# Performance work log

Measured on AMD Instinct MI355X. Metric: run time of the kernel, lower is better.

## Reference

```python
import jax, jax.numpy as jnp
import numpy as np

B, H, W, C = 64, 32, 32, 256
HZ, WZ = 16, 16
N = 64          # hidden_dim = n_proposals
K = 3           # dynamic depthwise kernel size
EPS = 1e-5


def _layernorm(x, g, b):
    mu = jnp.mean(x, axis=-1, keepdims=True)
    var = jnp.var(x, axis=-1, keepdims=True)
    return (x - mu) * jax.lax.rsqrt(var + EPS) * g + b


def setup_inputs() -> dict:
    key = jax.random.key(0)
    ks = jax.random.split(key, 8)
    s = 0.02  # weight init scale
    return {
        "x_feat": jax.random.normal(ks[0], (B, H, W, C), jnp.float32),
        "z_feat": jax.random.normal(ks[1], (B, HZ, WZ, C), jnp.float32),
        "Wz": jax.random.normal(ks[2], (C, N), jnp.float32) * s,
        "bz": jnp.zeros((N,), jnp.float32),
        "Wx": jax.random.normal(ks[3], (C, N), jnp.float32) * s,
        "bx": jnp.zeros((N,), jnp.float32),
        "Wdyn": jax.random.normal(ks[4], (C, N + K), jnp.float32) * s,
        "bdyn": jnp.zeros((N + K,), jnp.float32),
        "g_norm": jnp.ones((C,), jnp.float32),
        "b_norm": jnp.zeros((C,), jnp.float32),
        "Wp": jax.random.normal(ks[5], (C, 1), jnp.float32) * s,
        "bp": jnp.zeros((1,), jnp.float32),
        "g_ln": jnp.ones((C,), jnp.float32),
        "b_ln": jnp.zeros((C,), jnp.float32),
    }


def _dysep_conv_atten(query, value, Wdyn, bdyn, g_norm, b_norm):
    # query, value: [B, N, C]
    dy = query @ Wdyn + bdyn                      # [B, N, N+K]
    w_depth = dy[:, :, :K]                        # [B, N, K] per-channel depthwise kernels
    w_point = dy[:, :, K:]                        # [B, N, N] per-sample pointwise (1x1) weights
    # depthwise conv along C with 'same' padding (torch conv1d = cross-correlation)
    vpad = jnp.pad(value, ((0, 0), (0, 0), (1, 1)))
    depth = (w_depth[..., 0:1] * vpad[:, :, 0:C]
             + w_depth[..., 1:2] * vpad[:, :, 1:C + 1]
             + w_depth[..., 2:3] * vpad[:, :, 2:C + 2])
    depth = jax.nn.relu(depth)                    # [B, N, C]
    point = jnp.einsum('bnm,bmc->bnc', w_point, depth)
    return _layernorm(point, g_norm, b_norm)


def reference(x_feat, z_feat, Wz, bz, Wx, bx, Wdyn, bdyn,
              g_norm, b_norm, Wp, bp, g_ln, b_ln):
    # kernels from template features (detached in the original: kernels.detach())
    z_core = z_feat @ Wz + bz                                   # [B,HZ,WZ,N]
    kernels = jnp.einsum('bhwn,bhwc->bnc', z_core, z_feat)      # [B,N,C]
    kernels = jax.lax.stop_gradient(kernels)

    x_n = x_feat @ Wx + bx                                      # [B,H,W,N]
    kernels_x = jnp.einsum('bhwn,bhwc->bnc', x_n, x_feat)       # [B,N,C]
    kernels_x = _dysep_conv_atten(kernels, kernels_x, Wdyn, bdyn, g_norm, b_norm)

    x_corr = jnp.einsum('bnc,bhwn->bhwc', kernels_x, x_n)       # [B,H,W,C]
    proto = kernels_x @ Wp + bp                                 # [B,N,1]
    tem = jax.nn.sigmoid(jnp.einsum('bnd,bnc->bdc', proto, kernels_x))  # [B,1,C]
    tem = tem[:, :, None, :]                                    # [B,1,1,C]
    x_corr = x_corr * tem

    return x_feat + jax.nn.relu(_layernorm(x_corr, g_ln, b_ln))
```

## Files before the change

kernel.cpp:

```cpp
#include <hip/hip_runtime.h>
#include <math.h>

#define EPSV 1e-5f

typedef __attribute__((ext_vector_type(8))) short short8;
typedef __attribute__((ext_vector_type(4))) float f32x4;

static __device__ __forceinline__ unsigned bfpack2(float lo, float hi) {
    union { float f; unsigned u; } a, b;
    a.f = lo; b.f = hi;
    unsigned ua = a.u + 0x7fffu + ((a.u >> 16) & 1u);
    unsigned ub = b.u + 0x7fffu + ((b.u >> 16) & 1u);
    return (ua >> 16) | (ub & 0xffff0000u);
}

__global__ __launch_bounds__(256) void gram(
    const float* __restrict__ Xx, const float* __restrict__ Xz,
    float* __restrict__ Gx, float* __restrict__ Gz,
    float* __restrict__ csx, float* __restrict__ csz)
{
    __shared__ __align__(16) unsigned short AT[128 * 72];
    __shared__ __align__(16) unsigned short BT[128 * 72];
    __shared__ float csr[8 * 128];
    int id = blockIdx.x;
    const float* X; float* G; float* cs; int P;
    if (id < 192) { X = Xx; G = Gx; cs = csx; P = 1024; }
    else { id -= 192; X = Xz; G = Gz; cs = csz; P = 256; }
    const int b = id & 63;
    const int tile = id >> 6;
    const int ci = (tile == 1) ? 1 : 0;
    const int cj = (tile == 0) ? 0 : 1;
    const bool diag = (tile < 2);
    const int nk = P >> 6;
    const int t = threadIdx.x;
    const int cq = (t & 31) * 4;
    const int ph = t >> 5;
    const float* Xb = X + (long)b * P * 256;

    const int w = t >> 6;
    const int wr = w >> 1, wc = w & 1;
    const int quad = (t >> 4) & 3, lane16 = t & 15;

    f32x4 acc[4][4] = {};
    float csA[4] = {0.f, 0.f, 0.f, 0.f};

    for (int kc = 0; kc < nk; ++kc) {
        const int p0 = kc * 64 + ph * 8;
        float4 va[8], vb[8];
#pragma unroll
        for (int k = 0; k < 8; ++k)
            va[k] = *(const float4*)(Xb + (long)(p0 + k) * 256 + ci * 128 + cq);
        if (!diag) {
#pragma unroll
            for (int k = 0; k < 8; ++k)
                vb[k] = *(const float4*)(Xb + (long)(p0 + k) * 256 + cj * 128 + cq);
        }
        __syncthreads();
#pragma unroll
        for (int j = 0; j < 4; ++j) {
            uint4 pk;
            pk.x = bfpack2(((const float*)&va[0])[j], ((const float*)&va[1])[j]);
            pk.y = bfpack2(((const float*)&va[2])[j], ((const float*)&va[3])[j]);
            pk.z = bfpack2(((const float*)&va[4])[j], ((const float*)&va[5])[j]);
            pk.w = bfpack2(((const float*)&va[6])[j], ((const float*)&va[7])[j]);
            *(uint4*)&AT[(cq + j) * 72 + ph * 8] = pk;
            if (diag) {
                csA[j] += ((const float*)&va[0])[j] + ((const float*)&va[1])[j]
                        + ((const float*)&va[2])[j] + ((const float*)&va[3])[j]
                        + ((const float*)&va[4])[j] + ((const float*)&va[5])[j]
                        + ((const float*)&va[6])[j] + ((const float*)&va[7])[j];
            }
        }
        if (!diag) {
#pragma unroll
            for (int j = 0; j < 4; ++j) {
                uint4 pk;
                pk.x = bfpack2(((const float*)&vb[0])[j], ((const float*)&vb[1])[j]);
                pk.y = bfpack2(((const float*)&vb[2])[j], ((const float*)&vb[3])[j]);
                pk.z = bfpack2(((const float*)&vb[4])[j], ((const float*)&vb[5])[j]);
                pk.w = bfpack2(((const float*)&vb[6])[j], ((const float*)&vb[7])[j]);
                *(uint4*)&BT[(cq + j) * 72 + ph * 8] = pk;
            }
        }
        __syncthreads();
        const unsigned short* Br = diag ? AT : BT;
#pragma unroll
        for (int ks = 0; ks < 2; ++ks) {
            const int ko = ks * 32 + quad * 8;
            short8 bfrag[4];
#pragma unroll
            for (int ni = 0; ni < 4; ++ni)
                bfrag[ni] = *(const short8*)&Br[(wc * 64 + ni * 16 + lane16) * 72 + ko];
#pragma unroll
            for (int mi = 0; mi < 4; ++mi) {
                short8 afrag = *(const short8*)&AT[(wr * 64 + mi * 16 + lane16) * 72 + ko];
#pragma unroll
                for (int ni = 0; ni < 4; ++ni)
                    acc[mi][ni] = __builtin_amdgcn_mfma_f32_16x16x32_bf16(afrag, bfrag[ni], acc[mi][ni], 0, 0, 0);
            }
        }
    }
#pragma unroll
    for (int mi = 0; mi < 4; ++mi) {
        const int rbase = ci * 128 + wr * 64 + mi * 16 + quad * 4;
#pragma unroll
        for (int ni = 0; ni < 4; ++ni) {
            const int col = cj * 128 + wc * 64 + ni * 16 + lane16;
#pragma unroll
            for (int r = 0; r < 4; ++r) {
                G[((long)(b * 256 + rbase + r)) * 256 + col] = acc[mi][ni][r];
                if (!diag)
                    G[((long)(b * 256 + col)) * 256 + rbase + r] = acc[mi][ni][r];
            }
        }
    }
    if (diag) {
#pragma unroll
        for (int j = 0; j < 4; ++j) csr[ph * 128 + cq + j] = csA[j];
        __syncthreads();
        if (t < 128) {
            float s = 0.f;
#pragma unroll
            for (int k = 0; k < 8; ++k) s += csr[k * 128 + t];
            cs[b * 256 + ci * 128 + t] = s;
        }
    }
}

__global__ __launch_bounds__(256) void proj(
    const float* __restrict__ Gx, const float* __restrict__ csx,
    const float* __restrict__ Wx, const float* __restrict__ bx,
    float* __restrict__ kxr,
    const float* __restrict__ Gz, const float* __restrict__ csz,
    const float* __restrict__ Wz, const float* __restrict__ bz,
    float* __restrict__ kern)
{
    __shared__ __align__(16) unsigned short ATW[64 * 264];
    __shared__ __align__(16) unsigned short BTC[64 * 72];
    const int t = threadIdx.x;
    const int id = blockIdx.x;
    const int b = id & 63, s = id >> 6;
    const float *G, *cs, *W, *bias; float* O;
    if (s < 4) { G = Gx; cs = csx; W = Wx; bias = bx; O = kxr; }
    else       { G = Gz; cs = csz; W = Wz; bias = bz; O = kern; }
    const int ct = s & 3;
    const int n = t & 63, ph = t >> 6;
#pragma unroll
    for (int cc = 0; cc < 4; ++cc) {
        float v[16];
#pragma unroll
        for (int k = 0; k < 16; ++k) v[k] = W[(ph * 64 + cc * 16 + k) * 64 + n];
        uint4 p0, p1;
        p0.x = bfpack2(v[0], v[1]);   p0.y = bfpack2(v[2], v[3]);
        p0.z = bfpack2(v[4], v[5]);   p0.w = bfpack2(v[6], v[7]);
        p1.x = bfpack2(v[8], v[9]);   p1.y = bfpack2(v[10], v[11]);
        p1.z = bfpack2(v[12], v[13]); p1.w = bfpack2(v[14], v[15]);
        *(uint4*)&ATW[n * 264 + ph * 64 + cc * 16]     = p0;
        *(uint4*)&ATW[n * 264 + ph * 64 + cc * 16 + 8] = p1;
    }
    const int row = t >> 2, cq = t & 3;
    const int w = t >> 6, quad = (t >> 4) & 3, lane16 = t & 15;
    const float* Grow = G + ((long)(b * 256 + ct * 64 + row)) * 256 + cq * 16;
    f32x4 acc[4] = {{0.f,0.f,0.f,0.f},{0.f,0.f,0.f,0.f},{0.f,0.f,0.f,0.f},{0.f,0.f,0.f,0.f}};
    for (int kc = 0; kc < 4; ++kc) {
        float4 g0 = *(const float4*)(Grow + kc * 64 + 0);
        float4 g1 = *(const float4*)(Grow + kc * 64 + 4);
        float4 g2 = *(const float4*)(Grow + kc * 64 + 8);
        float4 g3 = *(const float4*)(Grow + kc * 64 + 12);
        uint4 pk0, pk1;
        pk0.x = bfpack2(g0.x, g0.y); pk0.y = bfpack2(g0.z, g0.w);
        pk0.z = bfpack2(g1.x, g1.y); pk0.w = bfpack2(g1.z, g1.w);
        pk1.x = bfpack2(g2.x, g2.y); pk1.y = bfpack2(g2.z, g2.w);
        pk1.z = bfpack2(g3.x, g3.y); pk1.w = bfpack2(g3.z, g3.w);
        __syncthreads();
        *(uint4*)&BTC[row * 72 + cq * 16]     = pk0;
        *(uint4*)&BTC[row * 72 + cq * 16 + 8] = pk1;
        __syncthreads();
#pragma unroll
        for (int ks = 0; ks < 2; ++ks) {
            const int ko = ks * 32 + quad * 8;
            short8 bfrag = *(const short8*)&BTC[(w * 16 + lane16) * 72 + ko];
#pragma unroll
            for (int mi = 0; mi < 4; ++mi) {
                short8 afrag = *(const short8*)&ATW[(mi * 16 + lane16) * 264 + kc * 64 + ko];
                acc[mi] = __builtin_amdgcn_mfma_f32_16x16x32_bf16(afrag, bfrag, acc[mi], 0, 0, 0);
            }
        }
    }
    const int col = ct * 64 + w * 16 + lane16;
    const float csv = cs[b * 256 + col];
#pragma unroll
    for (int mi = 0; mi < 4; ++mi) {
        const int nrow = mi * 16 + quad * 4;
#pragma unroll
        for (int r = 0; r < 4; ++r)
            O[((long)(b * 64 + nrow + r)) * 256 + col] = acc[mi][r] + bias[nrow + r] * csv;
    }
}

__global__ __launch_bounds__(256) void dy_all(
    const float* __restrict__ kern, const float* __restrict__ Wdyn,
    const float* __restrict__ bdyn, float* __restrict__ dyb)
{
    __shared__ float Ac[16 * 64];
    __shared__ float Wc[16 * 64];
    __shared__ float Wd3[48];
    const int b = blockIdx.x, t = threadIdx.x;
    const int tr = t >> 4, tc = t & 15;
    float acc[4][4];
#pragma unroll
    for (int j = 0; j < 4; ++j) {
        float bj = bdyn[3 + tc * 4 + j];
        acc[0][j] = bj; acc[1][j] = bj; acc[2][j] = bj; acc[3][j] = bj;
    }
    const int lr = t >> 2, lc = (t & 3) * 4;
    const int wl = t >> 4, wj = (t & 15) * 4;
    const int nwd = t / 3, jwd = t - nwd * 3;
    float wdacc = 0.f;
    float4 av = *(const float4*)(kern + ((long)(b * 64 + lr)) * 256 + lc);
    float w0 = Wdyn[wl * 67 + 3 + wj + 0];
    float w1 = Wdyn[wl * 67 + 3 + wj + 1];
    float w2 = Wdyn[wl * 67 + 3 + wj + 2];
    float w3 = Wdyn[wl * 67 + 3 + wj + 3];
    float wdr = (t < 48) ? Wdyn[(t / 3) * 67 + (t % 3)] : 0.f;

    for (int c0 = 0; c0 < 256; c0 += 16) {
        Ac[(lc+0)*64 + lr] = av.x; Ac[(lc+1)*64 + lr] = av.y;
        Ac[(lc+2)*64 + lr] = av.z; Ac[(lc+3)*64 + lr] = av.w;
        Wc[wl*64 + wj+0] = w0; Wc[wl*64 + wj+1] = w1;
        Wc[wl*64 + wj+2] = w2; Wc[wl*64 + wj+3] = w3;
        if (t < 48) Wd3[t] = wdr;
        __syncthreads();
        if (c0 + 16 < 256) {
            av = *(const float4*)(kern + ((long)(b * 64 + lr)) * 256 + c0 + 16 + lc);
            w0 = Wdyn[(c0 + 16 + wl) * 67 + 3 + wj + 0];
            w1 = Wdyn[(c0 + 16 + wl) * 67 + 3 + wj + 1];
            w2 = Wdyn[(c0 + 16 + wl) * 67 + 3 + wj + 2];
            w3 = Wdyn[(c0 + 16 + wl) * 67 + 3 + wj + 3];
            if (t < 48) wdr = Wdyn[(c0 + 16 + t / 3) * 67 + (t % 3)];
        }
#pragma unroll
        for (int cl = 0; cl < 16; ++cl) {
            float4 a = *(float4*)&Ac[cl * 64 + tr * 4];
            float4 w = *(float4*)&Wc[cl * 64 + tc * 4];
            acc[0][0]+=a.x*w.x; acc[0][1]+=a.x*w.y; acc[0][2]+=a.x*w.z; acc[0][3]+=a.x*w.w;
            acc[1][0]+=a.y*w.x; acc[1][1]+=a.y*w.y; acc[1][2]+=a.y*w.z; acc[1][3]+=a.y*w.w;
            acc[2][0]+=a.z*w.x; acc[2][1]+=a.z*w.y; acc[2][2]+=a.z*w.z; acc[2][3]+=a.z*w.w;
            acc[3][0]+=a.w*w.x; acc[3][1]+=a.w*w.y; acc[3][2]+=a.w*w.z; acc[3][3]+=a.w*w.w;
        }
        if (t < 192) {
#pragma unroll
            for (int cl = 0; cl < 16; ++cl)
                wdacc += Ac[cl * 64 + nwd] * Wd3[cl * 3 + jwd];
        }
        __syncthreads();
    }
#pragma unroll
    for (int i = 0; i < 4; ++i) {
        float4 o = make_float4(acc[i][0], acc[i][1], acc[i][2], acc[i][3]);
        *(float4*)(dyb + ((long)(b * 64 + tr * 4 + i)) * 68 + tc * 4) = o;
    }
    if (t < 192) dyb[((long)(b * 64 + nwd)) * 68 + 64 + jwd] = wdacc + bdyn[jwd];
}

__global__ __launch_bounds__(256) void depthpoint(
    const float* __restrict__ dyb, const float* __restrict__ v,
    const float* __restrict__ g, const float* __restrict__ Wp,
    float* __restrict__ point, float* __restrict__ partials)
{
    __shared__ float smem[13312];
    float* wpT = smem;
    float* wd3 = smem + 4352;
    float* vt  = smem + 4608;
    float* dep = smem + 8960;
    float* rs  = vt;

    const int t = threadIdx.x;
    const int b = blockIdx.y, ct = blockIdx.x, c0 = ct * 64;
    const int tr = t >> 4, tc = t & 15;

#pragma unroll
    for (int i = 0; i < 4; ++i) {
        int idx = t + i * 256; int n = idx >> 4, m0 = (idx & 15) * 4;
        float4 w4 = *(const float4*)(dyb + ((long)(b * 64 + n)) * 68 + m0);
        wpT[(m0+0)*68 + n] = w4.x; wpT[(m0+1)*68 + n] = w4.y;
        wpT[(m0+2)*68 + n] = w4.z; wpT[(m0+3)*68 + n] = w4.w;
    }
    if (t < 64) {
        long o = ((long)(b * 64 + t)) * 68 + 64;
        wd3[t*4+0] = dyb[o+0]; wd3[t*4+1] = dyb[o+1]; wd3[t*4+2] = dyb[o+2];
    }
    {
        int m = t >> 2, lc0 = (t & 3) * 17;
#pragma unroll
        for (int k = 0; k < 17; ++k) {
            int lc = lc0 + k;
            if (lc < 66) {
                int c = c0 - 1 + lc;
                vt[m * 68 + lc] = (c >= 0 && c < 256) ? v[((long)(b * 64 + m)) * 256 + c] : 0.f;
            }
        }
    }
    __syncthreads();
#pragma unroll
    for (int im = 0; im < 4; ++im) {
        int m = tr * 4 + im;
        float w0 = wd3[m*4+0], w1 = wd3[m*4+1], w2 = wd3[m*4+2];
#pragma unroll
        for (int jc = 0; jc < 4; ++jc) {
            int cl = tc * 4 + jc;
            float d = w0 * vt[m*68 + cl] + w1 * vt[m*68 + cl + 1] + w2 * vt[m*68 + cl + 2];
            dep[m*68 + cl] = fmaxf(d, 0.f);
        }
    }
    __syncthreads();
    float acc[4][4] = {};
#pragma unroll 16
    for (int m = 0; m < 64; ++m) {
        float4 a4 = *(float4*)&wpT[m * 68 + tr * 4];
        float4 d4 = *(float4*)&dep[m * 68 + tc * 4];
        acc[0][0]+=a4.x*d4.x; acc[0][1]+=a4.x*d4.y; acc[0][2]+=a4.x*d4.z; acc[0][3]+=a4.x*d4.w;
        acc[1][0]+=a4.y*d4.x; acc[1][1]+=a4.y*d4.y; acc[1][2]+=a4.y*d4.z; acc[1][3]+=a4.y*d4.w;
        acc[2][0]+=a4.z*d4.x; acc[2][1]+=a4.z*d4.y; acc[2][2]+=a4.z*d4.z; acc[2][3]+=a4.z*d4.w;
        acc[3][0]+=a4.w*d4.x; acc[3][1]+=a4.w*d4.y; acc[3][2]+=a4.w*d4.z; acc[3][3]+=a4.w*d4.w;
    }
    int cg = c0 + tc * 4;
    float4 g4  = *(const float4*)(g + cg);
    float4 wp4 = *(const float4*)(Wp + cg);
    float gw0 = g4.x*wp4.x, gw1 = g4.y*wp4.y, gw2 = g4.z*wp4.z, gw3 = g4.w*wp4.w;
#pragma unroll
    for (int i = 0; i < 4; ++i) {
        float4 o = make_float4(acc[i][0], acc[i][1], acc[i][2], acc[i][3]);
        *(float4*)(point + ((long)(b * 64 + tr * 4 + i)) * 256 + cg) = o;
        float s  = o.x + o.y + o.z + o.w;
        float s2 = o.x*o.x + o.y*o.y + o.z*o.z + o.w*o.w;
        float dg = o.x*gw0 + o.y*gw1 + o.z*gw2 + o.w*gw3;
        rs[0*1088 + (tr*4+i)*17 + tc] = s;
        rs[1*1088 + (tr*4+i)*17 + tc] = s2;
        rs[2*1088 + (tr*4+i)*17 + tc] = dg;
    }
    __syncthreads();
    if (t < 64) {
        float s = 0.f, s2 = 0.f, dg = 0.f;
#pragma unroll
        for (int j = 0; j < 16; ++j) {
            s  += rs[t*17 + j];
            s2 += rs[1088 + t*17 + j];
            dg += rs[2176 + t*17 + j];
        }
        long base = ((long)(b * 4 + ct)) * 192;
        partials[base + t]        = s;
        partials[base + 64 + t]   = s2;
        partials[base + 128 + t]  = dg;
    }
}

__global__ __launch_bounds__(256) void lntem(
    const float* __restrict__ partials, const float* __restrict__ point,
    const float* __restrict__ g, const float* __restrict__ bta,
    const float* __restrict__ Wp, const float* __restrict__ bp,
    float* __restrict__ murr, float* __restrict__ AB)
{
    __shared__ float sA[256], sB[256];
    __shared__ float wnv[64];
    __shared__ float tot[4];
    const int b = blockIdx.x, t = threadIdx.x;
    const int c = t;
    float gc = g[c], bc = bta[c], wpc = Wp[c];
    sA[t] = gc * wpc; sB[t] = bc * wpc;
    __syncthreads();
    for (int off = 128; off >= 1; off >>= 1) {
        if (t < off) { sA[t] += sA[t+off]; sB[t] += sB[t+off]; }
        __syncthreads();
    }
    if (t == 0) { tot[0] = sA[0]; tot[1] = sB[0] + bp[0]; }
    __syncthreads();
    float Sgw = tot[0], Sbw = tot[1];

    float protoe = 0.f, mu = 0.f, rr = 0.f;
    if (t < 64) {
        float S1 = 0.f, S2 = 0.f, Sdg = 0.f;
#pragma unroll
        for (int ct = 0; ct < 4; ++ct) {
            long o = ((long)(b * 4 + ct)) * 192;
            S1 += partials[o + t]; S2 += partials[o + 64 + t]; Sdg += partials[o + 128 + t];
        }
        mu = S1 * (1.f / 256.f);
        float var = S2 * (1.f / 256.f) - mu * mu;
        rr = rsqrtf(var + EPSV);
        protoe = rr * (Sdg - mu * Sgw) + Sbw;
        wnv[t] = protoe * rr;
        murr[b * 128 + 2*t]     = rr;
        murr[b * 128 + 2*t + 1] = -mu * rr;
    }
    __syncthreads();
    sA[t] = (t < 64) ? protoe * rr * mu : 0.f;
    sB[t] = (t < 64) ? protoe : 0.f;
    __syncthreads();
    for (int off = 128; off >= 1; off >>= 1) {
        if (t < off) { sA[t] += sA[t+off]; sB[t] += sB[t+off]; }
        __syncthreads();
    }
    if (t == 0) { tot[2] = sA[0]; tot[3] = sB[0]; }
    __syncthreads();
    float Bv = tot[2], Sv = tot[3];

    const float* pcol = point + (long)b * 64 * 256 + c;
    float a0 = 0.f, a1 = 0.f, a2 = 0.f, a3 = 0.f;
#pragma unroll
    for (int n = 0; n < 64; n += 4) {
        a0 += wnv[n+0] * pcol[(n+0) * 256];
        a1 += wnv[n+1] * pcol[(n+1) * 256];
        a2 += wnv[n+2] * pcol[(n+2) * 256];
        a3 += wnv[n+3] * pcol[(n+3) * 256];
    }
    float accA = a0 + a1 + a2 + a3;
    float x = gc * (accA - Bv) + bc * Sv;
    float temv = 1.f / (1.f + expf(-x));
    AB[b * 512 + c]       = gc * temv;
    AB[b * 512 + 256 + c] = bc * temv;
}

__global__ __launch_bounds__(256) void buildM(
    const float* __restrict__ point, const float* __restrict__ murr,
    const float* __restrict__ AB, const float* __restrict__ Wx,
    const float* __restrict__ bx,
    unsigned short* __restrict__ MT, float* __restrict__ svec)
{
    __shared__ float ks_s[64 * 68];
    __shared__ float wt_s[64 * 68];
    const int t = threadIdx.x;
    const int id = blockIdx.x;
    const int b = id & 63, mt = id >> 6;
    {
        const int n = t >> 2, q = t & 3;
        const float rn = murr[b * 128 + 2 * n], qn = murr[b * 128 + 2 * n + 1];
        const float* prow = point + ((long)(b * 64 + n)) * 256 + mt * 64 + q * 16;
        const float* Arow = AB + b * 512 + mt * 64 + q * 16;
#pragma unroll
        for (int j = 0; j < 4; ++j) {
            float4 p4 = *(const float4*)(prow + j * 4);
            float4 A4 = *(const float4*)(Arow + j * 4);
            float4 B4 = *(const float4*)(Arow + 256 + j * 4);
            float4 kv;
            kv.x = (p4.x * rn + qn) * A4.x + B4.x;
            kv.y = (p4.y * rn + qn) * A4.y + B4.y;
            kv.z = (p4.z * rn + qn) * A4.z + B4.z;
            kv.w = (p4.w * rn + qn) * A4.w + B4.w;
            *(float4*)&ks_s[n * 68 + q * 16 + j * 4] = kv;
        }
    }
    __syncthreads();
    if (t < 64) {
        float sv = 0.f;
#pragma unroll
        for (int n2 = 0; n2 < 64; ++n2) sv += bx[n2] * ks_s[n2 * 68 + t];
        svec[b * 256 + mt * 64 + t] = sv;
    }
    const int tr = t >> 4, tc = t & 15;
    const int nw = t & 63, ph = t >> 6;
    for (int cc = 0; cc < 4; ++cc) {
        float wv[16];
#pragma unroll
        for (int k = 0; k < 16; ++k) wv[k] = Wx[(cc * 64 + ph * 16 + k) * 64 + nw];
        __syncthreads();
#pragma unroll
        for (int k = 0; k < 16; ++k) wt_s[nw * 68 + ph * 16 + k] = wv[k];
        __syncthreads();
        float a2[4][4] = {};
#pragma unroll 16
        for (int n2 = 0; n2 < 64; ++n2) {
            float4 a4 = *(float4*)&ks_s[n2 * 68 + tr * 4];
            float4 w4 = *(float4*)&wt_s[n2 * 68 + tc * 4];
            a2[0][0]+=a4.x*w4.x; a2[0][1]+=a4.x*w4.y; a2[0][2]+=a4.x*w4.z; a2[0][3]+=a4.x*w4.w;
            a2[1][0]+=a4.y*w4.x; a2[1][1]+=a4.y*w4.y; a2[1][2]+=a4.y*w4.z; a2[1][3]+=a4.y*w4.w;
            a2[2][0]+=a4.z*w4.x; a2[2][1]+=a4.z*w4.y; a2[2][2]+=a4.z*w4.z; a2[2][3]+=a4.z*w4.w;
            a2[3][0]+=a4.w*w4.x; a2[3][1]+=a4.w*w4.y; a2[3][2]+=a4.w*w4.z; a2[3][3]+=a4.w*w4.w;
        }
#pragma unroll
        for (int i = 0; i < 4; ++i) {
            uint2 pk;
            pk.x = bfpack2(a2[i][0], a2[i][1]);
            pk.y = bfpack2(a2[i][2], a2[i][3]);
            *(uint2*)&MT[((long)(b * 256 + mt * 64 + tr * 4 + i)) * 256 + cc * 64 + tc * 4] = pk;
        }
    }
}

__global__ __launch_bounds__(256) void final2(
    const float* __restrict__ xf, const unsigned short* __restrict__ MT,
    const float* __restrict__ svec, const float* __restrict__ g,
    const float* __restrict__ bt, float* __restrict__ out)
{
    __shared__ __align__(16) float SlArr[32 * 132];
    __shared__ float red1[128], red2[128];
    __shared__ float muS[32], rrS[32];
    unsigned short* XT = (unsigned short*)SlArr;
    float* Sl = SlArr;
    const int t = threadIdx.x;
    const int id = blockIdx.x;
    const int b = id & 63, pt = id >> 6;
    const int w = t >> 6, quad = (t >> 4) & 3, lane16 = t & 15;
    const float* Xb = xf + ((long)(b * 1024 + pt * 32)) * 256;
    {
        const int p = t >> 3, q = t & 7;
#pragma unroll
        for (int i = 0; i < 8; ++i) {
            const int c = q * 32 + i * 4;
            float4 v = *(const float4*)(Xb + (long)p * 256 + c);
            uint2 pk;
            pk.x = bfpack2(v.x, v.y);
            pk.y = bfpack2(v.z, v.w);
            *(uint2*)&XT[p * 264 + c] = pk;
        }
    }
    __syncthreads();
    f32x4 acc[2][4] = {};
    const unsigned short* Mb = MT + (long)b * 65536;
    for (int ks = 0; ks < 8; ++ks) {
        const int ko = ks * 32 + quad * 8;
        short8 bf4[4], af2[2];
#pragma unroll
        for (int ni = 0; ni < 4; ++ni)
            bf4[ni] = *(const short8*)(Mb + (long)(w * 64 + ni * 16 + lane16) * 256 + ko);
#pragma unroll
        for (int mi = 0; mi < 2; ++mi)
            af2[mi] = *(const short8*)&XT[(mi * 16 + lane16) * 264 + ko];
#pragma unroll
        for (int mi = 0; mi < 2; ++mi)
#pragma unroll
            for (int ni = 0; ni < 4; ++ni)
                acc[mi][ni] = __builtin_amdgcn_mfma_f32_16x16x32_bf16(af2[mi], bf4[ni], acc[mi][ni], 0, 0, 0);
    }
    float sv4[4];
#pragma unroll
    for (int ni = 0; ni < 4; ++ni) sv4[ni] = svec[b * 256 + w * 64 + ni * 16 + lane16];
#pragma unroll
    for (int mi = 0; mi < 2; ++mi)
#pragma unroll
        for (int r = 0; r < 4; ++r) {
            float s1 = 0.f, s2 = 0.f;
#pragma unroll
            for (int ni = 0; ni < 4; ++ni) {
                float v2 = acc[mi][ni][r] + sv4[ni];
                acc[mi][ni][r] = v2;
                s1 += v2; s2 += v2 * v2;
            }
#pragma unroll
            for (int m = 1; m <= 8; m <<= 1) {
                s1 += __shfl_xor(s1, m);
                s2 += __shfl_xor(s2, m);
            }
            if (lane16 == 0) {
                red1[(mi * 16 + quad * 4 + r) * 4 + w] = s1;
                red2[(mi * 16 + quad * 4 + r) * 4 + w] = s2;
            }
        }
    __syncthreads();
    if (t < 32) {
        float sa = red1[t*4] + red1[t*4+1] + red1[t*4+2] + red1[t*4+3];
        float sb = red2[t*4] + red2[t*4+1] + red2[t*4+2] + red2[t*4+3];
        float m = sa * (1.f / 256.f);
        muS[t] = m;
        rrS[t] = rsqrtf(sb * (1.f / 256.f) - m * m + EPSV);
    }
#pragma unroll
    for (int h = 0; h < 2; ++h) {
        __syncthreads();
        if ((w >> 1) == h) {
            const int chalf = (w & 1) * 64;
#pragma unroll
            for (int mi = 0; mi < 2; ++mi)
#pragma unroll
                for (int ni = 0; ni < 4; ++ni)
#pragma unroll
                    for (int r = 0; r < 4; ++r)
                        Sl[(mi * 16 + quad * 4 + r) * 132 + chalf + ni * 16 + lane16] = acc[mi][ni][r];
        }
        __syncthreads();
        {
            const int p = t >> 3, q = t & 7;
            const float m = muS[p], rr = rrS[p];
            const long grow = ((long)(b * 1024 + pt * 32 + p)) * 256;
#pragma unroll
            for (int j = 0; j < 4; ++j) {
                const int cl = q * 16 + j * 4;
                const int c = h * 128 + cl;
                float4 a  = *(float4*)&Sl[p * 132 + cl];
                float4 g4 = *(const float4*)(g + c);
                float4 b4 = *(const float4*)(bt + c);
                float4 xv = *(const float4*)(xf + grow + c);
                float4 o;
                o.x = xv.x + fmaxf((a.x - m) * rr * g4.x + b4.x, 0.f);
                o.y = xv.y + fmaxf((a.y - m) * rr * g4.y + b4.y, 0.f);
                o.z = xv.z + fmaxf((a.z - m) * rr * g4.z + b4.z, 0.f);
                o.w = xv.w + fmaxf((a.w - m) * rr * g4.w + b4.w, 0.f);
                *(float4*)(out + grow + c) = o;
            }
        }
    }
}

extern "C" void kernel_launch(void* const* d_in, const int* in_sizes, int n_in,
                              void* d_out, int out_size, void* d_ws, size_t ws_size,
                              hipStream_t stream)
{
    (void)in_sizes; (void)n_in; (void)out_size; (void)ws_size;
    const float* x_feat = (const float*)d_in[0];
    const float* z_feat = (const float*)d_in[1];
    const float* Wz     = (const float*)d_in[2];
    const float* bz     = (const float*)d_in[3];
    const float* Wx     = (const float*)d_in[4];
    const float* bx     = (const float*)d_in[5];
    const float* Wdyn   = (const float*)d_in[6];
    const float* bdyn   = (const float*)d_in[7];
    const float* g_norm = (const float*)d_in[8];
    const float* b_norm = (const float*)d_in[9];
    const float* Wp     = (const float*)d_in[10];
    const float* bp     = (const float*)d_in[11];
    const float* g_ln   = (const float*)d_in[12];
    const float* b_ln   = (const float*)d_in[13];
    float* out = (float*)d_out;

    float* ws       = (float*)d_ws;
    float* Gx       = ws;
    float* Gz       = Gx + 4194304;
    float* kern     = Gz + 4194304;
    float* kxr      = kern + 1048576;
    float* point    = kxr + 1048576;
    float* dyb      = point + 1048576;
    float* partials = dyb + 278528;
    float* murr     = partials + 49152;
    float* AB       = murr + 8192;
    float* csx      = AB + 32768;
    float* csz      = csx + 16384;
    float* svec     = csz + 16384;
    unsigned short* MT = (unsigned short*)(svec + 16384);

    gram<<<384, 256, 0, stream>>>(x_feat, z_feat, Gx, Gz, csx, csz);
    proj<<<512, 256, 0, stream>>>(Gx, csx, Wx, bx, kxr, Gz, csz, Wz, bz, kern);
    dy_all<<<64, 256, 0, stream>>>(kern, Wdyn, bdyn, dyb);
    depthpoint<<<dim3(4, 64), 256, 0, stream>>>(dyb, kxr, g_norm, Wp, point, partials);
    lntem<<<64, 256, 0, stream>>>(partials, point, g_norm, b_norm, Wp, bp, murr, AB);
    buildM<<<256, 256, 0, stream>>>(point, murr, AB, Wx, bx, MT, svec);
    final2<<<2048, 256, 0, stream>>>(x_feat, MT, svec, g_ln, b_ln, out);
}
```

Before: 297.8 us.

## Store Gram matrices in bf16, fuse dynamic-weight GEMM into proj, swizzle gram LDS

Gram kernel now runs 512 threads with XOR-swizzled LDS tiles and writes bf16 Gram matrices, splitting the off-diagonal tile so each half-block writes one orientation instead of transposed scattered stores. Proj reads bf16 G fragments directly into registers, dropping the LDS staging and syncs. The z-path now also computes per-channel-slice partial products with Wdyn, which removes the serial 64-block dy_all kernel, and depthpoint sums the four partials plus bias. final2 prefetches the next MT fragments one step ahead. The aim is to cut memory traffic and a kernel launch, at the cost of extra bf16 rounding of G and extra partial-buffer traffic.

After: 280.0 us. -6.0%, faster.

```diff
diff --git a/kernel.cpp b/kernel.cpp
--- a/kernel.cpp
+++ b/kernel.cpp
@@ -13,258 +13,274 @@
     unsigned ub = b.u + 0x7fffu + ((b.u >> 16) & 1u);
     return (ua >> 16) | (ub & 0xffff0000u);
 }
-
-__global__ __launch_bounds__(256) void gram(
+static __device__ __forceinline__ unsigned short bf1(float v) {
+    return (unsigned short)bfpack2(v, 0.f);
+}
+
+__global__ __launch_bounds__(512) void gram(
     const float* __restrict__ Xx, const float* __restrict__ Xz,
-    float* __restrict__ Gx, float* __restrict__ Gz,
+    unsigned short* __restrict__ Gx, unsigned short* __restrict__ Gz,
     float* __restrict__ csx, float* __restrict__ csz)
 {
     __shared__ __align__(16) unsigned short AT[128 * 72];
     __shared__ __align__(16) unsigned short BT[128 * 72];
-    __shared__ float csr[8 * 128];
-    int id = blockIdx.x;
-    const float* X; float* G; float* cs; int P;
-    if (id < 192) { X = Xx; G = Gx; cs = csx; P = 1024; }
-    else { id -= 192; X = Xz; G = Gz; cs = csz; P = 256; }
+    __shared__ float csr[16 * 128];
+    const int id = blockIdx.x;
     const int b = id & 63;
-    const int tile = id >> 6;
-    const int ci = (tile == 1) ? 1 : 0;
-    const int cj = (tile == 0) ? 0 : 1;
+    const int path = (id >> 6) & 1;
+    const int tile = id >> 7;
     const bool diag = (tile < 2);
+    const int ci = diag ? tile : 0;
+    const float* X = path ? Xz : Xx;
+    unsigned short* G = (path ? Gz : Gx) + (long)b * 65536;
+    float* cs = path ? csz : csx;
+    const int P = path ? 256 : 1024;
     const int nk = P >> 6;
     const int t = threadIdx.x;
     const int cq = (t & 31) * 4;
     const int ph = t >> 5;
+    const int w = t >> 6;
+    const int quad = (t >> 4) & 3, lane16 = t & 15;
     const float* Xb = X + (long)b * P * 256;
-
-    const int w = t >> 6;
-    const int wr = w >> 1, wc = w & 1;
-    const int quad = (t >> 4) & 3, lane16 = t & 15;
+    const int colA = ci * 128;
 
     f32x4 acc[4][4] = {};
     float csA[4] = {0.f, 0.f, 0.f, 0.f};
 
     for (int kc = 0; kc < nk; ++kc) {
-        const int p0 = kc * 64 + ph * 8;
-        float4 va[8], vb[8];
-#pragma unroll
-        for (int k = 0; k < 8; ++k)
-            va[k] = *(const float4*)(Xb + (long)(p0 + k) * 256 + ci * 128 + cq);
+        const int p0 = kc * 64 + ph * 4;
+        float4 va[4], vb[4];
+#pragma unroll
+        for (int k = 0; k < 4; ++k)
+            va[k] = *(const float4*)(Xb + (long)(p0 + k) * 256 + colA + cq);
         if (!diag) {
 #pragma unroll
-            for (int k = 0; k < 8; ++k)
-                vb[k] = *(const float4*)(Xb + (long)(p0 + k) * 256 + cj * 128 + cq);
+            for (int k = 0; k < 4; ++k)
+                vb[k] = *(const float4*)(Xb + (long)(p0 + k) * 256 + 128 + cq);
         }
         __syncthreads();
 #pragma unroll
         for (int j = 0; j < 4; ++j) {
-            uint4 pk;
+            const int row = cq + j;
+            const int key = (row >> 2) & 7;
+            uint2 pk;
             pk.x = bfpack2(((const float*)&va[0])[j], ((const float*)&va[1])[j]);
             pk.y = bfpack2(((const float*)&va[2])[j], ((const float*)&va[3])[j]);
-            pk.z = bfpack2(((const float*)&va[4])[j], ((const float*)&va[5])[j]);
-            pk.w = bfpack2(((const float*)&va[6])[j], ((const float*)&va[7])[j]);
-            *(uint4*)&AT[(cq + j) * 72 + ph * 8] = pk;
-            if (diag) {
+            *(uint2*)&AT[row * 72 + (((ph >> 1) ^ key) << 3) + ((ph & 1) << 2)] = pk;
+            if (diag)
                 csA[j] += ((const float*)&va[0])[j] + ((const float*)&va[1])[j]
-                        + ((const float*)&va[2])[j] + ((const float*)&va[3])[j]
-                        + ((const float*)&va[4])[j] + ((const float*)&va[5])[j]
-                        + ((const float*)&va[6])[j] + ((const float*)&va[7])[j];
-            }
+                        + ((const float*)&va[2])[j] + ((const float*)&va[3])[j];
         }
         if (!diag) {
 #pragma unroll
             for (int j = 0; j < 4; ++j) {
-                uint4 pk;
+                const int row = cq + j;
+                const int key = (row >> 2) & 7;
+                uint2 pk;
                 pk.x = bfpack2(((const float*)&vb[0])[j], ((const float*)&vb[1])[j]);
                 pk.y = bfpack2(((const float*)&vb[2])[j], ((const float*)&vb[3])[j]);
-                pk.z = bfpack2(((const float*)&vb[4])[j], ((const float*)&vb[5])[j]);
-                pk.w = bfpack2(((const float*)&vb[6])[j], ((const float*)&vb[7])[j]);
-                *(uint4*)&BT[(cq + j) * 72 + ph * 8] = pk;
-            }
-        }
-        __syncthreads();
-        const unsigned short* Br = diag ? AT : BT;
-#pragma unroll
-        for (int ks = 0; ks < 2; ++ks) {
-            const int ko = ks * 32 + quad * 8;
-            short8 bfrag[4];
-#pragma unroll
-            for (int ni = 0; ni < 4; ++ni)
-                bfrag[ni] = *(const short8*)&Br[(wc * 64 + ni * 16 + lane16) * 72 + ko];
-#pragma unroll
-            for (int mi = 0; mi < 4; ++mi) {
-                short8 afrag = *(const short8*)&AT[(wr * 64 + mi * 16 + lane16) * 72 + ko];
-#pragma unroll
-                for (int ni = 0; ni < 4; ++ni)
-                    acc[mi][ni] = __builtin_amdgcn_mfma_f32_16x16x32_bf16(afrag, bfrag[ni], acc[mi][ni], 0, 0, 0);
-            }
-        }
-    }
-#pragma unroll
-    for (int mi = 0; mi < 4; ++mi) {
-        const int rbase = ci * 128 + wr * 64 + mi * 16 + quad * 4;
-#pragma unroll
-        for (int ni = 0; ni < 4; ++ni) {
-            const int col = cj * 128 + wc * 64 + ni * 16 + lane16;
-#pragma unroll
-            for (int r = 0; r < 4; ++r) {
-                G[((long)(b * 256 + rbase + r)) * 256 + col] = acc[mi][ni][r];
-                if (!diag)
-                    G[((long)(b * 256 + col)) * 256 + rbase + r] = acc[mi][ni][r];
+                *(uint2*)&BT[row * 72 + (((ph >> 1) ^ key) << 3) + ((ph & 1) << 2)] = pk;
+            }
+        }
+        __syncthreads();
+        if (diag) {
+            const int wr = w >> 2, wc4 = w & 3;
+#pragma unroll
+            for (int ks = 0; ks < 2; ++ks) {
+                const int slot = ks * 4 + quad;
+                short8 bfr[2];
+#pragma unroll
+                for (int ni = 0; ni < 2; ++ni) {
+                    const int rw = wc4 * 32 + ni * 16 + lane16;
+                    bfr[ni] = *(const short8*)&AT[rw * 72 + ((slot ^ ((rw >> 2) & 7)) << 3)];
+                }
+#pragma unroll
+                for (int mi = 0; mi < 4; ++mi) {
+                    const int ra = wr * 64 + mi * 16 + lane16;
+                    short8 afr = *(const short8*)&AT[ra * 72 + ((slot ^ ((ra >> 2) & 7)) << 3)];
+#pragma unroll
+                    for (int ni = 0; ni < 2; ++ni)
+                        acc[mi][ni] = __builtin_amdgcn_mfma_f32_16x16x32_bf16(afr, bfr[ni], acc[mi][ni], 0, 0, 0);
+                }
+            }
+        } else {
+            const int sel = w >> 2, w2 = w & 3, wr = w2 >> 1, wc = w2 & 1;
+            const unsigned short* As = sel ? BT : AT;
+            const unsigned short* Bs = sel ? AT : BT;
+#pragma unroll
+            for (int ks = 0; ks < 2; ++ks) {
+                const int slot = ks * 4 + quad;
+                short8 bfr[4];
+#pragma unroll
+                for (int ni = 0; ni < 4; ++ni) {
+                    const int rw = wc * 64 + ni * 16 + lane16;
+                    bfr[ni] = *(const short8*)&Bs[rw * 72 + ((slot ^ ((rw >> 2) & 7)) << 3)];
+                }
+#pragma unroll
+                for (int mi = 0; mi < 4; ++mi) {
+                    const int ra = wr * 64 + mi * 16 + lane16;
+                    short8 afr = *(const short8*)&As[ra * 72 + ((slot ^ ((ra >> 2) & 7)) << 3)];
+#pragma unroll
+                    for (int ni = 0; ni < 4; ++ni)
+                        acc[mi][ni] = __builtin_amdgcn_mfma_f32_16x16x32_bf16(afr, bfr[ni], acc[mi][ni], 0, 0, 0);
+                }
             }
         }
     }
     if (diag) {
+        const int wr = w >> 2, wc4 = w & 3;
+#pragma unroll
+        for (int mi = 0; mi < 4; ++mi) {
+            const int rbase = ci * 128 + wr * 64 + mi * 16 + quad * 4;
+#pragma unroll
+            for (int ni = 0; ni < 2; ++ni) {
+                const int col = ci * 128 + wc4 * 32 + ni * 16 + lane16;
+#pragma unroll
+                for (int r = 0; r < 4; ++r)
+                    G[(rbase + r) * 256 + col] = bf1(acc[mi][ni][r]);
+            }
+        }
 #pragma unroll
         for (int j = 0; j < 4; ++j) csr[ph * 128 + cq + j] = csA[j];
         __syncthreads();
         if (t < 128) {
             float s = 0.f;
 #pragma unroll
-            for (int k = 0; k < 8; ++k) s += csr[k * 128 + t];
+            for (int k = 0; k < 16; ++k) s += csr[k * 128 + t];
             cs[b * 256 + ci * 128 + t] = s;
         }
+    } else {
+        const int sel = w >> 2, w2 = w & 3, wr = w2 >> 1, wc = w2 & 1;
+        const int R = sel ? 128 : 0, C = sel ? 0 : 128;
+#pragma unroll
+        for (int mi = 0; mi < 4; ++mi) {
+            const int rbase = R + wr * 64 + mi * 16 + quad * 4;
+#pragma unroll
+            for (int ni = 0; ni < 4; ++ni) {
+                const int col = C + wc * 64 + ni * 16 + lane16;
+#pragma unroll
+                for (int r = 0; r < 4; ++r)
+                    G[(rbase + r) * 256 + col] = bf1(acc[mi][ni][r]);
+            }
+        }
     }
 }
 
 __global__ __launch_bounds__(256) void proj(
-    const float* __restrict__ Gx, const float* __restrict__ csx,
+    const unsigned short* __restrict__ Gx, const float* __restrict__ csx,
     const float* __restrict__ Wx, const float* __restrict__ bx,
     float* __restrict__ kxr,
-    const float* __restrict__ Gz, const float* __restrict__ csz,
+    const unsigned short* __restrict__ Gz, const float* __restrict__ csz,
     const float* __restrict__ Wz, const float* __restrict__ bz,
-    float* __restrict__ kern)
+    const float* __restrict__ Wdyn, float* __restrict__ dypart)
 {
     __shared__ __align__(16) unsigned short ATW[64 * 264];
-    __shared__ __align__(16) unsigned short BTC[64 * 72];
+    __shared__ float SLICE[64 * 68];
+    __shared__ float WC2[64 * 68];
+    __shared__ float WD3L[192];
     const int t = threadIdx.x;
     const int id = blockIdx.x;
     const int b = id & 63, s = id >> 6;
-    const float *G, *cs, *W, *bias; float* O;
-    if (s < 4) { G = Gx; cs = csx; W = Wx; bias = bx; O = kxr; }
-    else       { G = Gz; cs = csz; W = Wz; bias = bz; O = kern; }
+    const bool xp = (s < 4);
     const int ct = s & 3;
-    const int n = t & 63, ph = t >> 6;
+    const unsigned short* G = xp ? Gx : Gz;
+    const float* cs   = xp ? csx : csz;
+    const float* W    = xp ? Wx : Wz;
+    const float* bias = xp ? bx : bz;
+    const int n = t & 63, ph2 = t >> 6;
 #pragma unroll
     for (int cc = 0; cc < 4; ++cc) {
         float v[16];
 #pragma unroll
-        for (int k = 0; k < 16; ++k) v[k] = W[(ph * 64 + cc * 16 + k) * 64 + n];
+        for (int k = 0; k < 16; ++k) v[k] = W[(ph2 * 64 + cc * 16 + k) * 64 + n];
         uint4 p0, p1;
         p0.x = bfpack2(v[0], v[1]);   p0.y = bfpack2(v[2], v[3]);
         p0.z = bfpack2(v[4], v[5]);   p0.w = bfpack2(v[6], v[7]);
         p1.x = bfpack2(v[8], v[9]);   p1.y = bfpack2(v[10], v[11]);
         p1.z = bfpack2(v[12], v[13]); p1.w = bfpack2(v[14], v[15]);
-        *(uint4*)&ATW[n * 264 + ph * 64 + cc * 16]     = p0;
-        *(uint4*)&ATW[n * 264 + ph * 64 + cc * 16 + 8] = p1;
-    }
-    const int row = t >> 2, cq = t & 3;
+        *(uint4*)&ATW[n * 264 + ph2 * 64 + cc * 16]     = p0;
+        *(uint4*)&ATW[n * 264 + ph2 * 64 + cc * 16 + 8] = p1;
+    }
+    __syncthreads();
     const int w = t >> 6, quad = (t >> 4) & 3, lane16 = t & 15;
-    const float* Grow = G + ((long)(b * 256 + ct * 64 + row)) * 256 + cq * 16;
+    const unsigned short* Grow =
+        G + (long)(b * 256 + ct * 64 + w * 16 + lane16) * 256 + quad * 8;
+    short8 bfr[8];
+#pragma unroll
+    for (int u = 0; u < 8; ++u) bfr[u] = *(const short8*)(Grow + u * 32);
     f32x4 acc[4] = {{0.f,0.f,0.f,0.f},{0.f,0.f,0.f,0.f},{0.f,0.f,0.f,0.f},{0.f,0.f,0.f,0.f}};
-    for (int kc = 0; kc < 4; ++kc) {
-        float4 g0 = *(const float4*)(Grow + kc * 64 + 0);
-        float4 g1 = *(const float4*)(Grow + kc * 64 + 4);
-        float4 g2 = *(const float4*)(Grow + kc * 64 + 8);
-        float4 g3 = *(const float4*)(Grow + kc * 64 + 12);
-        uint4 pk0, pk1;
-        pk0.x = bfpack2(g0.x, g0.y); pk0.y = bfpack2(g0.z, g0.w);
-        pk0.z = bfpack2(g1.x, g1.y); pk0.w = bfpack2(g1.z, g1.w);
-        pk1.x = bfpack2(g2.x, g2.y); pk1.y = bfpack2(g2.z, g2.w);
-        pk1.z = bfpack2(g3.x, g3.y); pk1.w = bfpack2(g3.z, g3.w);
-        __syncthreads();
-        *(uint4*)&BTC[row * 72 + cq * 16]     = pk0;
-        *(uint4*)&BTC[row * 72 + cq * 16 + 8] = pk1;
-        __syncthreads();
+#pragma unroll
+    for (int kc = 0; kc < 4; ++kc)
 #pragma unroll
         for (int ks = 0; ks < 2; ++ks) {
             const int ko = ks * 32 + quad * 8;
-            short8 bfrag = *(const short8*)&BTC[(w * 16 + lane16) * 72 + ko];
+            const short8 bfrag = bfr[kc * 2 + ks];
 #pragma unroll
             for (int mi = 0; mi < 4; ++mi) {
                 short8 afrag = *(const short8*)&ATW[(mi * 16 + lane16) * 264 + kc * 64 + ko];
                 acc[mi] = __builtin_amdgcn_mfma_f32_16x16x32_bf16(afrag, bfrag, acc[mi], 0, 0, 0);
             }
         }
-    }
     const int col = ct * 64 + w * 16 + lane16;
     const float csv = cs[b * 256 + col];
-#pragma unroll
-    for (int mi = 0; mi < 4; ++mi) {
-        const int nrow = mi * 16 + quad * 4;
-#pragma unroll
-        for (int r = 0; r < 4; ++r)
-            O[((long)(b * 64 + nrow + r)) * 256 + col] = acc[mi][r] + bias[nrow + r] * csv;
-    }
-}
-
-__global__ __launch_bounds__(256) void dy_all(
-    const float* __restrict__ kern, const float* __restrict__ Wdyn,
-    const float* __restrict__ bdyn, float* __restrict__ dyb)
-{
-    __shared__ float Ac[16 * 64];
-    __shared__ float Wc[16 * 64];
-    __shared__ float Wd3[48];
-    const int b = blockIdx.x, t = threadIdx.x;
-    const int tr = t >> 4, tc = t & 15;
-    float acc[4][4];
-#pragma unroll
-    for (int j = 0; j < 4; ++j) {
-        float bj = bdyn[3 + tc * 4 + j];
-        acc[0][j] = bj; acc[1][j] = bj; acc[2][j] = bj; acc[3][j] = bj;
-    }
-    const int lr = t >> 2, lc = (t & 3) * 4;
-    const int wl = t >> 4, wj = (t & 15) * 4;
-    const int nwd = t / 3, jwd = t - nwd * 3;
-    float wdacc = 0.f;
-    float4 av = *(const float4*)(kern + ((long)(b * 64 + lr)) * 256 + lc);
-    float w0 = Wdyn[wl * 67 + 3 + wj + 0];
-    float w1 = Wdyn[wl * 67 + 3 + wj + 1];
-    float w2 = Wdyn[wl * 67 + 3 + wj + 2];
-    float w3 = Wdyn[wl * 67 + 3 + wj + 3];
-    float wdr = (t < 48) ? Wdyn[(t / 3) * 67 + (t % 3)] : 0.f;
-
-    for (int c0 = 0; c0 < 256; c0 += 16) {
-        Ac[(lc+0)*64 + lr] = av.x; Ac[(lc+1)*64 + lr] = av.y;
-        Ac[(lc+2)*64 + lr] = av.z; Ac[(lc+3)*64 + lr] = av.w;
-        Wc[wl*64 + wj+0] = w0; Wc[wl*64 + wj+1] = w1;
-        Wc[wl*64 + wj+2] = w2; Wc[wl*64 + wj+3] = w3;
-        if (t < 48) Wd3[t] = wdr;
-        __syncthreads();
-        if (c0 + 16 < 256) {
-            av = *(const float4*)(kern + ((long)(b * 64 + lr)) * 256 + c0 + 16 + lc);
-            w0 = Wdyn[(c0 + 16 + wl) * 67 + 3 + wj + 0];
-            w1 = Wdyn[(c0 + 16 + wl) * 67 + 3 + wj + 1];
-            w2 = Wdyn[(c0 + 16 + wl) * 67 + 3 + wj + 2];
-            w3 = Wdyn[(c0 + 16 + wl) * 67 + 3 + wj + 3];
-            if (t < 48) wdr = Wdyn[(c0 + 16 + t / 3) * 67 + (t % 3)];
-        }
-#pragma unroll
-        for (int cl = 0; cl < 16; ++cl) {
-            float4 a = *(float4*)&Ac[cl * 64 + tr * 4];
-            float4 w = *(float4*)&Wc[cl * 64 + tc * 4];
-            acc[0][0]+=a.x*w.x; acc[0][1]+=a.x*w.y; acc[0][2]+=a.x*w.z; acc[0][3]+=a.x*w.w;
-            acc[1][0]+=a.y*w.x; acc[1][1]+=a.y*w.y; acc[1][2]+=a.y*w.z; acc[1][3]+=a.y*w.w;
-            acc[2][0]+=a.z*w.x; acc[2][1]+=a.z*w.y; acc[2][2]+=a.z*w.z; acc[2][3]+=a.z*w.w;
-            acc[3][0]+=a.w*w.x; acc[3][1]+=a.w*w.y; acc[3][2]+=a.w*w.z; acc[3][3]+=a.w*w.w;
+    if (xp) {
+#pragma unroll
+        for (int mi = 0; mi < 4; ++mi) {
+            const int nrow = mi * 16 + quad * 4;
+#pragma unroll
+            for (int r = 0; r < 4; ++r)
+                kxr[((long)(b * 64 + nrow + r)) * 256 + col] = acc[mi][r] + bias[nrow + r] * csv;
+        }
+    } else {
+        const int cloc = w * 16 + lane16;
+#pragma unroll
+        for (int mi = 0; mi < 4; ++mi) {
+            const int nrow = mi * 16 + quad * 4;
+#pragma unroll
+            for (int r = 0; r < 4; ++r)
+                SLICE[cloc * 68 + nrow + r] = acc[mi][r] + bias[nrow + r] * csv;
+        }
+        {
+            const int m = t & 63, clg = t >> 6;
+#pragma unroll
+            for (int j = 0; j < 16; ++j) {
+                const int cl = clg * 16 + j;
+                WC2[cl * 68 + m] = Wdyn[((long)(ct * 64 + cl)) * 67 + 3 + m];
+            }
+            if (t < 192) WD3L[t] = Wdyn[((long)(ct * 64 + t / 3)) * 67 + (t % 3)];
+        }
+        __syncthreads();
+        const int tr = t >> 4, tc = t & 15;
+        float adv[4][4] = {};
+#pragma unroll 16
+        for (int cl = 0; cl < 64; ++cl) {
+            float4 a  = *(float4*)&SLICE[cl * 68 + tr * 4];
+            float4 wv = *(float4*)&WC2[cl * 68 + tc * 4];
+            adv[0][0]+=a.x*wv.x; adv[0][1]+=a.x*wv.y; adv[0][2]+=a.x*wv.z; adv[0][3]+=a.x*wv.w;
+            adv[1][0]+=a.y*wv.x; adv[1][1]+=a.y*wv.y; adv[1][2]+=a.y*wv.z; adv[1][3]+=a.y*wv.w;
+            adv[2][0]+=a.z*wv.x; adv[2][1]+=a.z*wv.y; adv[2][2]+=a.z*wv.z; adv[2][3]+=a.z*wv.w;
+            adv[3][0]+=a.w*wv.x; adv[3][1]+=a.w*wv.y; adv[3][2]+=a.w*wv.z; adv[3][3]+=a.w*wv.w;
+        }
+        const long base = (long)(b * 4 + ct) * 64;
+#pragma unroll
+        for (int i = 0; i < 4; ++i) {
+            float4 o = make_float4(adv[i][0], adv[i][1], adv[i][2], adv[i][3]);
+            *(float4*)(dypart + (base + tr * 4 + i) * 68 + tc * 4) = o;
         }
         if (t < 192) {
-#pragma unroll
-            for (int cl = 0; cl < 16; ++cl)
-                wdacc += Ac[cl * 64 + nwd] * Wd3[cl * 3 + jwd];
-        }
-        __syncthreads();
-    }
-#pragma unroll
-    for (int i = 0; i < 4; ++i) {
-        float4 o = make_float4(acc[i][0], acc[i][1], acc[i][2], acc[i][3]);
-        *(float4*)(dyb + ((long)(b * 64 + tr * 4 + i)) * 68 + tc * 4) = o;
-    }
-    if (t < 192) dyb[((long)(b * 64 + nwd)) * 68 + 64 + jwd] = wdacc + bdyn[jwd];
+            const int nwd3 = t / 3, jwd3 = t - nwd3 * 3;
+            float wdacc = 0.f;
+#pragma unroll 16
+            for (int cl = 0; cl < 64; ++cl)
+                wdacc += SLICE[cl * 68 + nwd3] * WD3L[cl * 3 + jwd3];
+            dypart[(base + nwd3) * 68 + 64 + jwd3] = wdacc;
+        }
+    }
 }
 
 __global__ __launch_bounds__(256) void depthpoint(
-    const float* __restrict__ dyb, const float* __restrict__ v,
+    const float* __restrict__ dyp, const float* __restrict__ bdyn,
+    const float* __restrict__ v,
     const float* __restrict__ g, const float* __restrict__ Wp,
     float* __restrict__ point, float* __restrict__ partials)
 {
@@ -282,13 +298,26 @@
 #pragma unroll
     for (int i = 0; i < 4; ++i) {
         int idx = t + i * 256; int n = idx >> 4, m0 = (idx & 15) * 4;
-        float4 w4 = *(const float4*)(dyb + ((long)(b * 64 + n)) * 68 + m0);
+        float4 a0 = *(const float4*)(dyp + ((long)((b * 4 + 0) * 64 + n)) * 68 + m0);
+        float4 a1 = *(const float4*)(dyp + ((long)((b * 4 + 1) * 64 + n)) * 68 + m0);
+        float4 a2 = *(const float4*)(dyp + ((long)((b * 4 + 2) * 64 + n)) * 68 + m0);
+        float4 a3 = *(const float4*)(dyp + ((long)((b * 4 + 3) * 64 + n)) * 68 + m0);
+        float4 w4;
+        w4.x = a0.x + a1.x + a2.x + a3.x + bdyn[3 + m0 + 0];
+        w4.y = a0.y + a1.y + a2.y + a3.y + bdyn[3 + m0 + 1];
+        w4.z = a0.z + a1.z + a2.z + a3.z + bdyn[3 + m0 + 2];
+        w4.w = a0.w + a1.w + a2.w + a3.w + bdyn[3 + m0 + 3];
         wpT[(m0+0)*68 + n] = w4.x; wpT[(m0+1)*68 + n] = w4.y;
         wpT[(m0+2)*68 + n] = w4.z; wpT[(m0+3)*68 + n] = w4.w;
     }
     if (t < 64) {
-        long o = ((long)(b * 64 + t)) * 68 + 64;
-        wd3[t*4+0] = dyb[o+0]; wd3[t*4+1] = dyb[o+1]; wd3[t*4+2] = dyb[o+2];
+        long o0 = ((long)((b * 4 + 0) * 64 + t)) * 68 + 64;
+        long o1 = ((long)((b * 4 + 1) * 64 + t)) * 68 + 64;
+        long o2 = ((long)((b * 4 + 2) * 64 + t)) * 68 + 64;
+        long o3 = ((long)((b * 4 + 3) * 64 + t)) * 68 + 64;
+#pragma unroll
+        for (int j = 0; j < 3; ++j)
+            wd3[t*4+j] = dyp[o0+j] + dyp[o1+j] + dyp[o2+j] + dyp[o3+j] + bdyn[j];
     }
     {
         int m = t >> 2, lc0 = (t & 3) * 17;
@@ -516,13 +545,20 @@
     }
     __syncthreads();
     f32x4 acc[2][4] = {};
-    const unsigned short* Mb = MT + (long)b * 65536;
+    const unsigned short* Mb = MT + (long)b * 65536 + quad * 8;
+    short8 bf4[4];
+#pragma unroll
+    for (int ni = 0; ni < 4; ++ni)
+        bf4[ni] = *(const short8*)(Mb + (long)(w * 64 + ni * 16 + lane16) * 256);
     for (int ks = 0; ks < 8; ++ks) {
         const int ko = ks * 32 + quad * 8;
-        short8 bf4[4], af2[2];
-#pragma unroll
-        for (int ni = 0; ni < 4; ++ni)
-            bf4[ni] = *(const short8*)(Mb + (long)(w * 64 + ni * 16 + lane16) * 256 + ko);
+        short8 nbf[4];
+        if (ks + 1 < 8) {
+#pragma unroll
+            for (int ni = 0; ni < 4; ++ni)
+                nbf[ni] = *(const short8*)(Mb + (long)(w * 64 + ni * 16 + lane16) * 256 + (ks + 1) * 32);
+        }
+        short8 af2[2];
 #pragma unroll
         for (int mi = 0; mi < 2; ++mi)
             af2[mi] = *(const short8*)&XT[(mi * 16 + lane16) * 264 + ko];
@@ -531,6 +567,8 @@
 #pragma unroll
             for (int ni = 0; ni < 4; ++ni)
                 acc[mi][ni] = __builtin_amdgcn_mfma_f32_16x16x32_bf16(af2[mi], bf4[ni], acc[mi][ni], 0, 0, 0);
+#pragma unroll
+        for (int ni = 0; ni < 4; ++ni) bf4[ni] = nbf[ni];
     }
     float sv4[4];
 #pragma unroll
@@ -623,24 +661,24 @@
     float* out = (float*)d_out;
 
     float* ws       = (float*)d_ws;
-    float* Gx       = ws;
-    float* Gz       = Gx + 4194304;
-    float* kern     = Gz + 4194304;
-    float* kxr      = kern + 1048576;
+    float* kxr      = ws;
     float* point    = kxr + 1048576;
-    float* dyb      = point + 1048576;
-    float* partials = dyb + 278528;
+    float* dypart   = point + 1048576;
+    float* partials = dypart + 1114112;
     float* murr     = partials + 49152;
     float* AB       = murr + 8192;
     float* csx      = AB + 32768;
     float* csz      = csx + 16384;
     float* svec     = csz + 16384;
-    unsigned short* MT = (unsigned short*)(svec + 16384);
-
-    gram<<<384, 256, 0, stream>>>(x_feat, z_feat, Gx, Gz, csx, csz);
-    proj<<<512, 256, 0, stream>>>(Gx, csx, Wx, bx, kxr, Gz, csz, Wz, bz, kern);
-    dy_all<<<64, 256, 0, stream>>>(kern, Wdyn, bdyn, dyb);
-    depthpoint<<<dim3(4, 64), 256, 0, stream>>>(dyb, kxr, g_norm, Wp, point, partials);
+    unsigned short* Gx = (unsigned short*)(svec + 16384);
+    unsigned short* Gz = Gx + 4194304;
+    unsigned short* MT = Gz + 4194304;
+
+    gram<<<384, 512, 0, stream>>>(x_feat, z_feat, Gx, Gz, csx, csz);
+    proj<<<512, 256, 0, stream>>>(Gx, csx, Wx, bx, kxr, Gz, csz, Wz, bz,
+                                  Wdyn, dypart);
+    depthpoint<<<dim3(4, 64), 256, 0, stream>>>(dypart, bdyn, kxr, g_norm, Wp,
+                                                point, partials);
     lntem<<<64, 256, 0, stream>>>(partials, point, g_norm, b_norm, Wp, bp, murr, AB);
     buildM<<<256, 256, 0, stream>>>(point, murr, AB, Wx, bx, MT, svec);
     final2<<<2048, 256, 0, stream>>>(x_feat, MT, svec, g_ln, b_ln, out);
```
